# Performance work log

Hardware: AMD Instinct MI355X
Metric: run time of the kernel (lower is better)

The kernel has to match this reference:

```python
import jax, jax.numpy as jnp
import numpy as np

KERNEL_MUL = 2.0
KERNEL_NUM = 5
EPS = 1e-06
CLAMP_MAX = 50.0


def setup_inputs() -> dict:
    key = jax.random.key(0)
    k1, k2 = jax.random.split(key)
    B, D = 2048, 2048
    source = jax.random.normal(k1, (B, D), dtype=jnp.float32)
    target = jax.random.normal(k2, (B, D), dtype=jnp.float32)
    return {"source": source, "target": target}


def _mmd_rbf(source, target):
    B = source.shape[0]
    total = jnp.concatenate([source, target], axis=0)  # [2B, D]
    total = jnp.nan_to_num(total, nan=0.0, posinf=10000.0, neginf=-10000.0)
    # squared pairwise distances via |a|^2 + |b|^2 - 2 a.b (same math as (diff**2).sum(-1))
    sq = jnp.sum(total * total, axis=1)                       # [2B]
    L2 = sq[:, None] + sq[None, :] - 2.0 * (total @ total.T)  # [2B, 2B]
    L2 = jnp.maximum(L2, 0.0)
    # bandwidth: detached mean of L2, clamped
    bw = jax.lax.stop_gradient(jnp.maximum(jnp.mean(L2), EPS))
    kernels = jnp.zeros_like(L2)
    for i in range(KERNEL_NUM):
        bw_i = jnp.maximum(bw * (KERNEL_MUL ** i), EPS)
        scaled = jnp.minimum(L2 / bw_i, CLAMP_MAX)
        kernels = kernels + jnp.exp(-scaled)
    XX = jnp.mean(kernels[:B, :B])
    YY = jnp.mean(kernels[B:, B:])
    XY = jnp.mean(kernels[:B, B:])
    YX = jnp.mean(kernels[B:, :B])
    loss = XX + YY - XY - YX
    # auto_fallback: linear MMD (detached) if RBF loss is non-finite
    delta = jnp.mean(source, axis=0) - jnp.mean(target, axis=0)
    lin = jax.lax.stop_gradient(jnp.dot(delta, delta))
    return jnp.where(jnp.isfinite(loss), loss, lin)


def reference(source, target):
    return _mmd_rbf(source, target)
```

## Files before the change

### kernel.cpp

```cpp
#include <hip/hip_runtime.h>
#include <cstdint>
#include <cmath>

#define DD 2048
#define NROW 4096
#define BHALF 2048
#define NT 16

typedef __attribute__((ext_vector_type(4))) int i32x4;
typedef __attribute__((ext_vector_type(8))) signed char c8;

typedef __attribute__((address_space(1))) const void* as1cv;
typedef __attribute__((address_space(3))) void* as3v;

__device__ __forceinline__ void gload_lds16(const void* g, void* l) {
  __builtin_amdgcn_global_load_lds((as1cv)g, (as3v)l, 16, 0, 0);
}

__device__ __forceinline__ float fixv(float x) {
  if (isnan(x)) return 0.0f;
  if (isinf(x)) return x > 0.0f ? 10000.0f : -10000.0f;
  return x;
}

constexpr size_t TQ_OFF     = 0;
constexpr size_t SQ8_OFF    = (size_t)NROW * DD;
constexpr size_t CS_SRC_OFF = SQ8_OFF + NROW * 4;
constexpr size_t CS_TGT_OFF = CS_SRC_OFF + DD * 4;
constexpr size_t ACC_OFF    = CS_TGT_OFF + DD * 4;
constexpr size_t SCAL_OFF   = ACC_OFF + 4 * 8;
constexpr size_t CNT_OFF    = SCAL_OFF + 8;
constexpr size_t ZERO_BYTES = 16384 + 8192 + 8192 + 32 + 8 + 8;

__global__ __launch_bounds__(256) void k_prep(const float* __restrict__ src,
                                              const float* __restrict__ tgt,
                                              signed char* __restrict__ Tq,
                                              int* __restrict__ sq8,
                                              float* __restrict__ cs_src,
                                              float* __restrict__ cs_tgt) {
  int b = blockIdx.x;
  int rb = b >> 4, cb = b & 15;
  int t = threadIdx.x;
  int cl = t & 15;
  int rt = t >> 4;
  const float* base;
  float* csp;
  if (rb < 16) { base = src + (size_t)(rb * 128) * DD; csp = cs_src; }
  else         { base = tgt + (size_t)(rb - 16) * 128 * DD; csp = cs_tgt; }
  int c0 = cb * 128 + cl * 8;
  float cacc[8] = {0, 0, 0, 0, 0, 0, 0, 0};
  __shared__ float cpart[16][16][8];
#pragma unroll
  for (int pass = 0; pass < 8; ++pass) {
    int row = pass * 16 + rt;
    const float4* p = (const float4*)(base + (size_t)row * DD + c0);
    float4 v0 = p[0], v1 = p[1];
    float x[8] = {v0.x, v0.y, v0.z, v0.w, v1.x, v1.y, v1.z, v1.w};
    c8 qq;
    int a = 0;
#pragma unroll
    for (int j = 0; j < 8; ++j) {
      float f = fixv(x[j]);
      int qi = __float2int_rn(f * 16.0f);
      qi = max(-127, min(127, qi));
      a += qi * qi;
      cacc[j] += (float)qi;
      qq[j] = (signed char)qi;
    }
    *(c8*)(Tq + (size_t)(rb * 128 + row) * DD + c0) = qq;
    a += __shfl_xor(a, 1); a += __shfl_xor(a, 2);
    a += __shfl_xor(a, 4); a += __shfl_xor(a, 8);
    if (cl == 0) atomicAdd(&sq8[rb * 128 + row], a);
  }
#pragma unroll
  for (int j = 0; j < 8; ++j) cpart[rt][cl][j] = cacc[j];
  __syncthreads();
  if (t < 128) {
    int cl2 = t >> 3, j = t & 7;
    float s = 0.0f;
#pragma unroll
    for (int r2 = 0; r2 < 16; ++r2) s += cpart[r2][cl2][j];
    atomicAdd(&csp[cb * 128 + cl2 * 8 + j], s);
  }
}

__global__ __launch_bounds__(512, 2) void k_mmd(const signed char* __restrict__ Tq,
                                                const int* __restrict__ sq8,
                                                const float* __restrict__ cs_src,
                                                const float* __restrict__ cs_tgt,
                                                double* __restrict__ accd,
                                                float* __restrict__ scal,
                                                unsigned int* __restrict__ cnt,
                                                float* __restrict__ out) {
  int lin = blockIdx.x;
  int t5 = (lin & 7) * 32 + (lin >> 3);
  int bi = t5 >> 4, bj = t5 & 15;

  __shared__ __attribute__((aligned(16))) signed char Sb[131072];

  int tid = threadIdx.x, l = tid & 63, w = tid >> 6;
  int wr = w >> 2, wc = w & 3;
  int l15 = l & 15;

  i32x4 acc[8][4];
#pragma unroll
  for (int m = 0; m < 8; ++m)
#pragma unroll
    for (int n = 0; n < 4; ++n) acc[m][n] = (i32x4){0, 0, 0, 0};

  int colsw = ((l & 3) ^ ((l >> 3) & 3)) * 16;
  size_t gA0 = (size_t)(bi * 256 + w * 16 + (l >> 2)) * DD + colsw;
  size_t gB0 = (size_t)(bj * 256 + w * 16 + (l >> 2)) * DD + colsw;
  int dW = w * 1024;

#define CALLA(bf, kc, h, T) gload_lds16(                                        \
      Tq + gA0 + (size_t)(h) * 128 * DD + (size_t)(T) * 128 + (kc) * 64,        \
      (void*)(Sb + (bf) + (kc) * 32768 + (h) * 8192 + dW))
#define CALLB(bf, kc, h, T) gload_lds16(                                        \
      Tq + gB0 + (size_t)(h) * 128 * DD + (size_t)(T) * 128 + (kc) * 64,        \
      (void*)(Sb + (bf) + (kc) * 32768 + 16384 + (h) * 8192 + dW))

  int slotx = (((l >> 4) ^ ((l15 >> 1) & 3))) * 16;
  int aB = (wr * 128 + l15) * 64 + slotx;
  int bB = 16384 + (wc * 64 + l15) * 64 + slotx;

#define BAR()  __builtin_amdgcn_s_barrier()

#pragma unroll
  for (int kc = 0; kc < 2; ++kc)
#pragma unroll
    for (int h = 0; h < 2; ++h) { CALLA(0, kc, h, 0); CALLB(0, kc, h, 0); }
  asm volatile("s_waitcnt vmcnt(0)" ::: "memory");
  BAR();

#pragma unroll 1
  for (int t = 0; t < NT; ++t) {
    const int bf = (t & 1) << 16;
    const int ob = bf ^ 65536;
    i32x4 aF[4][2], bF[4][2];
#pragma unroll
    for (int kc = 0; kc < 2; ++kc) {
#pragma unroll
      for (int mi = 0; mi < 4; ++mi)
        aF[mi][kc] = *(const i32x4*)(Sb + bf + kc * 32768 + aB + mi * 1024);
#pragma unroll
      for (int n = 0; n < 4; ++n)
        bF[n][kc] = *(const i32x4*)(Sb + bf + kc * 32768 + bB + n * 1024);
    }
    if (t < NT - 1) {
#pragma unroll
      for (int kc = 0; kc < 2; ++kc)
#pragma unroll
        for (int h = 0; h < 2; ++h) { CALLA(ob, kc, h, t + 1); CALLB(ob, kc, h, t + 1); }
    }
    __builtin_amdgcn_s_setprio(1);
#pragma unroll
    for (int mi = 0; mi < 4; ++mi)
#pragma unroll
      for (int n = 0; n < 4; ++n)
#pragma unroll
        for (int kc = 0; kc < 2; ++kc)
          acc[mi][n] = __builtin_amdgcn_mfma_i32_16x16x64_i8(aF[mi][kc], bF[n][kc], acc[mi][n], 0, 0, 0);
    __builtin_amdgcn_s_setprio(0);
    i32x4 aG[4][2];
#pragma unroll
    for (int kc = 0; kc < 2; ++kc)
#pragma unroll
      for (int mi = 0; mi < 4; ++mi)
        aG[mi][kc] = *(const i32x4*)(Sb + bf + kc * 32768 + aB + (4 + mi) * 1024);
    __builtin_amdgcn_s_setprio(1);
#pragma unroll
    for (int mi = 0; mi < 4; ++mi)
#pragma unroll
      for (int n = 0; n < 4; ++n)
#pragma unroll
        for (int kc = 0; kc < 2; ++kc)
          acc[4 + mi][n] = __builtin_amdgcn_mfma_i32_16x16x64_i8(aG[mi][kc], bF[n][kc], acc[4 + mi][n], 0, 0, 0);
    __builtin_amdgcn_s_setprio(0);
    if (t < NT - 1) asm volatile("s_waitcnt vmcnt(0)" ::: "memory");
    BAR();
  }

  float* red = (float*)Sb;
  float bw;
  {
    float ssq = 0.0f, s2 = 0.0f, dl = 0.0f;
#pragma unroll
    for (int k2 = 0; k2 < 8; ++k2) ssq += (float)sq8[tid + k2 * 512];
#pragma unroll
    for (int k2 = 0; k2 < 4; ++k2) {
      int c = tid + k2 * 512;
      float a = cs_src[c], b2 = cs_tgt[c];
      float s = a + b2;
      s2 += s * s;
      float d = a - b2;
      dl += d * d;
    }
    for (int o = 32; o; o >>= 1) {
      ssq += __shfl_xor(ssq, o);
      s2  += __shfl_xor(s2, o);
      dl  += __shfl_xor(dl, o);
    }
    __syncthreads();
    if (l == 0) { red[w] = ssq; red[8 + w] = s2; red[16 + w] = dl; }
    __syncthreads();
    double S = 0.0, Q = 0.0;
#pragma unroll
    for (int i = 0; i < 8; ++i) { S += red[i]; Q += red[8 + i]; }
    double meanL2 = (2.0 * S / (double)NROW -
                     2.0 * Q / ((double)NROW * (double)NROW)) * (1.0 / 256.0);
    bw = (float)fmax(meanL2, 1e-6);
    if (tid == 0 && lin == 0) {
      double L = 0.0;
      for (int i = 0; i < 8; ++i) L += red[16 + i];
      scal[0] = (float)(L * (1.0 / (256.0 * 4194304.0)));
    }
  }

  float inv4 = 1.0f / fmaxf(bw * 16.0f, 1e-6f);

  float sum = 0.0f;
  int rbase = bi * 256 + wr * 128 + ((l >> 4) * 4);
  int cbase = bj * 256 + wc * 64 + l15;
#pragma unroll
  for (int m = 0; m < 8; ++m) {
    int4 sr = *(const int4*)(sq8 + rbase + m * 16);
    int sqr[4] = {sr.x, sr.y, sr.z, sr.w};
#pragma unroll
    for (int n = 0; n < 4; ++n) {
      int sc = sq8[cbase + n * 16];
#pragma unroll
      for (int r = 0; r < 4; ++r) {
        float L2 = (float)(sqr[r] + sc - 2 * acc[m][n][r]) * (1.0f / 256.0f);
        L2 = fmaxf(L2, 0.0f);
        float e4 = __expf(-L2 * inv4);
        float e3 = e4 * e4;
        float e2 = e3 * e3;
        float e1 = e2 * e2;
        float e0 = e1 * e1;
        sum += ((e0 + e1) + (e2 + e3)) + e4;
      }
    }
  }
  for (int o = 32; o; o >>= 1) sum += __shfl_xor(sum, o);
  if (l == 0) red[32 + w] = sum;
  __syncthreads();
  if (tid == 0) {
    double tot = 0.0;
    for (int i = 0; i < 8; ++i) tot += red[32 + i];
    int cat = (bi >= 8) * 2 + (bj >= 8);
    atomicAdd(accd + cat, tot);
    __threadfence();
    unsigned int old = atomicAdd(cnt, 1u);
    if (old == 255u) {
      __threadfence();
      double loss = (accd[0] + accd[3] - accd[1] - accd[2]) * (1.0 / 4194304.0);
      if (!isfinite(loss)) loss = (double)scal[0];
      out[0] = (float)loss;
    }
  }
}

extern "C" void kernel_launch(void* const* d_in, const int* in_sizes, int n_in,
                              void* d_out, int out_size, void* d_ws, size_t ws_size,
                              hipStream_t stream) {
  const float* src = (const float*)d_in[0];
  const float* tgt = (const float*)d_in[1];
  char* ws = (char*)d_ws;
  signed char* Tq  = (signed char*)(ws + TQ_OFF);
  int*    sq8    = (int*)(ws + SQ8_OFF);
  float*  cs_src = (float*)(ws + CS_SRC_OFF);
  float*  cs_tgt = (float*)(ws + CS_TGT_OFF);
  double* accd   = (double*)(ws + ACC_OFF);
  float*  scal   = (float*)(ws + SCAL_OFF);
  unsigned int* cnt = (unsigned int*)(ws + CNT_OFF);

  hipMemsetAsync(ws + SQ8_OFF, 0, ZERO_BYTES, stream);

  k_prep<<<512, 256, 0, stream>>>(src, tgt, Tq, sq8, cs_src, cs_tgt);
  k_mmd<<<256, 512, 0, stream>>>(Tq, sq8, cs_src, cs_tgt, accd, scal, cnt,
                                 (float*)d_out);
}
```

Measured before the change: 63.87 us.

## Exploit Gram symmetry: compute upper-triangle 128x128 tiles only, weighting off-diagonal blocks twice

Switches from a full 16x16 grid of 256x256 output tiles to the 528 upper-triangular tiles of a 32x32 grid of 128x128 tiles. The tile index is decoded with a sqrt formula plus correction loops. Off-diagonal tiles add their sum to both the (i,j) and (j,i) category accumulators. This roughly halves the int8 MFMA and exp work. The smaller tiles reduce LDS and accumulator registers, allowing 4 blocks per CU, but each tile reuses its loaded data less.

```diff
diff --git a/kernel.cpp b/kernel.cpp
--- a/kernel.cpp
+++ b/kernel.cpp
@@ -6,6 +6,8 @@
 #define NROW 4096
 #define BHALF 2048
 #define NT 16
+#define NB 32
+#define NTRI 528
 
 typedef __attribute__((ext_vector_type(4))) int i32x4;
 typedef __attribute__((ext_vector_type(8))) signed char c8;
@@ -84,7 +86,7 @@
   }
 }
 
-__global__ __launch_bounds__(512, 2) void k_mmd(const signed char* __restrict__ Tq,
+__global__ __launch_bounds__(512, 4) void k_mmd(const signed char* __restrict__ Tq,
                                                 const int* __restrict__ sq8,
                                                 const float* __restrict__ cs_src,
                                                 const float* __restrict__ cs_tgt,
@@ -93,89 +95,74 @@
                                                 unsigned int* __restrict__ cnt,
                                                 float* __restrict__ out) {
   int lin = blockIdx.x;
-  int t5 = (lin & 7) * 32 + (lin >> 3);
-  int bi = t5 >> 4, bj = t5 & 15;
-
-  __shared__ __attribute__((aligned(16))) signed char Sb[131072];
+  int t5 = (lin & 7) * (NTRI / 8) + (lin >> 3);
+  int bi = (int)((65.0 - sqrt(4225.0 - 8.0 * (double)t5)) * 0.5);
+  if (bi > NB - 1) bi = NB - 1;
+  while (32 * (bi + 1) - ((bi + 1) * bi) / 2 <= t5) ++bi;
+  while (32 * bi - (bi * (bi - 1)) / 2 > t5) --bi;
+  int bj = bi + (t5 - (32 * bi - (bi * (bi - 1)) / 2));
+
+  __shared__ __attribute__((aligned(16))) signed char Sb[65536];
 
   int tid = threadIdx.x, l = tid & 63, w = tid >> 6;
   int wr = w >> 2, wc = w & 3;
   int l15 = l & 15;
 
-  i32x4 acc[8][4];
-#pragma unroll
-  for (int m = 0; m < 8; ++m)
-#pragma unroll
-    for (int n = 0; n < 4; ++n) acc[m][n] = (i32x4){0, 0, 0, 0};
+  i32x4 acc[4][2];
+#pragma unroll
+  for (int m = 0; m < 4; ++m)
+#pragma unroll
+    for (int n = 0; n < 2; ++n) acc[m][n] = (i32x4){0, 0, 0, 0};
 
   int colsw = ((l & 3) ^ ((l >> 3) & 3)) * 16;
-  size_t gA0 = (size_t)(bi * 256 + w * 16 + (l >> 2)) * DD + colsw;
-  size_t gB0 = (size_t)(bj * 256 + w * 16 + (l >> 2)) * DD + colsw;
+  size_t gA0 = (size_t)(bi * 128 + w * 16 + (l >> 2)) * DD + colsw;
+  size_t gB0 = (size_t)(bj * 128 + w * 16 + (l >> 2)) * DD + colsw;
   int dW = w * 1024;
 
-#define CALLA(bf, kc, h, T) gload_lds16(                                        \
-      Tq + gA0 + (size_t)(h) * 128 * DD + (size_t)(T) * 128 + (kc) * 64,        \
-      (void*)(Sb + (bf) + (kc) * 32768 + (h) * 8192 + dW))
-#define CALLB(bf, kc, h, T) gload_lds16(                                        \
-      Tq + gB0 + (size_t)(h) * 128 * DD + (size_t)(T) * 128 + (kc) * 64,        \
-      (void*)(Sb + (bf) + (kc) * 32768 + 16384 + (h) * 8192 + dW))
+#define CALLA(bf, kc, T) gload_lds16(                                           \
+      Tq + gA0 + (size_t)(T) * 128 + (kc) * 64,                                 \
+      (void*)(Sb + (bf) + (kc) * 16384 + dW))
+#define CALLB(bf, kc, T) gload_lds16(                                           \
+      Tq + gB0 + (size_t)(T) * 128 + (kc) * 64,                                 \
+      (void*)(Sb + (bf) + (kc) * 16384 + 8192 + dW))
 
   int slotx = (((l >> 4) ^ ((l15 >> 1) & 3))) * 16;
-  int aB = (wr * 128 + l15) * 64 + slotx;
-  int bB = 16384 + (wc * 64 + l15) * 64 + slotx;
+  int aB = (wr * 64 + l15) * 64 + slotx;
+  int bB = 8192 + (wc * 32 + l15) * 64 + slotx;
 
 #define BAR()  __builtin_amdgcn_s_barrier()
 
 #pragma unroll
-  for (int kc = 0; kc < 2; ++kc)
-#pragma unroll
-    for (int h = 0; h < 2; ++h) { CALLA(0, kc, h, 0); CALLB(0, kc, h, 0); }
+  for (int kc = 0; kc < 2; ++kc) { CALLA(0, kc, 0); CALLB(0, kc, 0); }
   asm volatile("s_waitcnt vmcnt(0)" ::: "memory");
   BAR();
 
 #pragma unroll 1
   for (int t = 0; t < NT; ++t) {
-    const int bf = (t & 1) << 16;
-    const int ob = bf ^ 65536;
-    i32x4 aF[4][2], bF[4][2];
+    const int bf = (t & 1) << 15;
+    const int ob = bf ^ 32768;
+    i32x4 aF[4][2], bF[2][2];
 #pragma unroll
     for (int kc = 0; kc < 2; ++kc) {
 #pragma unroll
       for (int mi = 0; mi < 4; ++mi)
-        aF[mi][kc] = *(const i32x4*)(Sb + bf + kc * 32768 + aB + mi * 1024);
-#pragma unroll
-      for (int n = 0; n < 4; ++n)
-        bF[n][kc] = *(const i32x4*)(Sb + bf + kc * 32768 + bB + n * 1024);
+        aF[mi][kc] = *(const i32x4*)(Sb + bf + kc * 16384 + aB + mi * 1024);
+#pragma unroll
+      for (int ni = 0; ni < 2; ++ni)
+        bF[ni][kc] = *(const i32x4*)(Sb + bf + kc * 16384 + bB + ni * 1024);
     }
     if (t < NT - 1) {
 #pragma unroll
-      for (int kc = 0; kc < 2; ++kc)
-#pragma unroll
-        for (int h = 0; h < 2; ++h) { CALLA(ob, kc, h, t + 1); CALLB(ob, kc, h, t + 1); }
+      for (int kc = 0; kc < 2; ++kc) { CALLA(ob, kc, t + 1); CALLB(ob, kc, t + 1); }
     }
     __builtin_amdgcn_s_setprio(1);
 #pragma unroll
     for (int mi = 0; mi < 4; ++mi)
 #pragma unroll
-      for (int n = 0; n < 4; ++n)
+      for (int ni = 0; ni < 2; ++ni)
 #pragma unroll
         for (int kc = 0; kc < 2; ++kc)
-          acc[mi][n] = __builtin_amdgcn_mfma_i32_16x16x64_i8(aF[mi][kc], bF[n][kc], acc[mi][n], 0, 0, 0);
-    __builtin_amdgcn_s_setprio(0);
-    i32x4 aG[4][2];
-#pragma unroll
-    for (int kc = 0; kc < 2; ++kc)
-#pragma unroll
-      for (int mi = 0; mi < 4; ++mi)
-        aG[mi][kc] = *(const i32x4*)(Sb + bf + kc * 32768 + aB + (4 + mi) * 1024);
-    __builtin_amdgcn_s_setprio(1);
-#pragma unroll
-    for (int mi = 0; mi < 4; ++mi)
-#pragma unroll
-      for (int n = 0; n < 4; ++n)
-#pragma unroll
-        for (int kc = 0; kc < 2; ++kc)
-          acc[4 + mi][n] = __builtin_amdgcn_mfma_i32_16x16x64_i8(aG[mi][kc], bF[n][kc], acc[4 + mi][n], 0, 0, 0);
+          acc[mi][ni] = __builtin_amdgcn_mfma_i32_16x16x64_i8(aF[mi][kc], bF[ni][kc], acc[mi][ni], 0, 0, 0);
     __builtin_amdgcn_s_setprio(0);
     if (t < NT - 1) asm volatile("s_waitcnt vmcnt(0)" ::: "memory");
     BAR();
@@ -220,18 +207,18 @@
   float inv4 = 1.0f / fmaxf(bw * 16.0f, 1e-6f);
 
   float sum = 0.0f;
-  int rbase = bi * 256 + wr * 128 + ((l >> 4) * 4);
-  int cbase = bj * 256 + wc * 64 + l15;
-#pragma unroll
-  for (int m = 0; m < 8; ++m) {
-    int4 sr = *(const int4*)(sq8 + rbase + m * 16);
+  int rbase = bi * 128 + wr * 64 + ((l >> 4) * 4);
+  int cbase = bj * 128 + wc * 32 + l15;
+#pragma unroll
+  for (int mi = 0; mi < 4; ++mi) {
+    int4 sr = *(const int4*)(sq8 + rbase + mi * 16);
     int sqr[4] = {sr.x, sr.y, sr.z, sr.w};
 #pragma unroll
-    for (int n = 0; n < 4; ++n) {
-      int sc = sq8[cbase + n * 16];
+    for (int ni = 0; ni < 2; ++ni) {
+      int sc = sq8[cbase + ni * 16];
 #pragma unroll
       for (int r = 0; r < 4; ++r) {
-        float L2 = (float)(sqr[r] + sc - 2 * acc[m][n][r]) * (1.0f / 256.0f);
+        float L2 = (float)(sqr[r] + sc - 2 * acc[mi][ni][r]) * (1.0f / 256.0f);
         L2 = fmaxf(L2, 0.0f);
         float e4 = __expf(-L2 * inv4);
         float e3 = e4 * e4;
@@ -248,11 +235,15 @@
   if (tid == 0) {
     double tot = 0.0;
     for (int i = 0; i < 8; ++i) tot += red[32 + i];
-    int cat = (bi >= 8) * 2 + (bj >= 8);
+    int cat = (bi >= 16) * 2 + (bj >= 16);
     atomicAdd(accd + cat, tot);
+    if (bi != bj) {
+      int catT = (bj >= 16) * 2 + (bi >= 16);
+      atomicAdd(accd + catT, tot);
+    }
     __threadfence();
     unsigned int old = atomicAdd(cnt, 1u);
-    if (old == 255u) {
+    if (old == NTRI - 1) {
       __threadfence();
       double loss = (accd[0] + accd[3] - accd[1] - accd[2]) * (1.0 / 4194304.0);
       if (!isfinite(loss)) loss = (double)scal[0];
@@ -278,6 +269,6 @@
   hipMemsetAsync(ws + SQ8_OFF, 0, ZERO_BYTES, stream);
 
   k_prep<<<512, 256, 0, stream>>>(src, tgt, Tq, sq8, cs_src, cs_tgt);
-  k_mmd<<<256, 512, 0, stream>>>(Tq, sq8, cs_src, cs_tgt, accd, scal, cnt,
-                                 (float*)d_out);
-}
+  k_mmd<<<NTRI, 512, 0, stream>>>(Tq, sq8, cs_src, cs_tgt, accd, scal, cnt,
+                                  (float*)d_out);
+}
```

Result: slower. 70.61 us (+10.6%).
